# Kernel optimization log

Hardware: AMD Instinct MI355X
Metric: run time of the kernel (lower is better)

## Reference

```python
import jax, jax.numpy as jnp
import numpy as np
import math

STATE_DIM = 512
NUM_GROUPS = 32
VMD_MODES = 8
PERM_DIM = 4
MAX_PATTERNS = math.factorial(PERM_DIM)  # 24


def setup_inputs() -> dict:
    key = jax.random.key(0)
    B, T = 16, 4096
    hidden_states = jax.random.normal(key, (B, T, STATE_DIM), dtype=jnp.float32)
    return {"hidden_states": hidden_states}


def _vmd_decomposition(signals):
    # signals: [B, G, T] -> modes [B, G, K, T]
    B, G, T = signals.shape
    K = VMD_MODES
    fft_signal = jnp.fft.fft(signals, axis=2)
    freqs = jnp.fft.fftfreq(T).astype(jnp.float32)
    bandwidth = 1.0 / K
    center_freqs = jnp.linspace(-0.5, 0.5, K, dtype=jnp.float32)
    dist = jnp.abs(freqs[None, :] - center_freqs[:, None])          # [K, T]
    filters = jnp.exp(-0.5 * (dist / bandwidth) ** 2)
    filtered = fft_signal[:, :, None, :] * filters[None, None, :, :]
    return jnp.fft.ifft(filtered, axis=3).real.astype(jnp.float32)


def _pattern_ids(windows):
    # windows: [B, G, K, N, m] -> Lehmer-code pattern ids [B, G, K, N]
    m = windows.shape[-1]
    si = jnp.argsort(windows, axis=-1)
    fact = [math.factorial(j) for j in range(m)]
    pid = jnp.zeros(windows.shape[:-1], dtype=jnp.int32)
    for i in range(m - 1):
        smaller = (si[..., i:i + 1] > si[..., i + 1:]).sum(axis=-1).astype(jnp.int32)
        pid = pid + smaller * fact[m - 1 - i]
    return pid


def _tmptm(modes):
    # modes: [B, G, K, T] -> normalized transition histogram [B, G, MP^2]
    B, G, K, T = modes.shape
    m, MP = PERM_DIM, MAX_PATTERNS
    N = T - m + 1
    # unfold(3, m, 1): [B, G, K, N, m]
    windows = jnp.stack([modes[..., i:i + N] for i in range(m)], axis=-1)
    pid = _pattern_ids(windows)                       # [B, G, K, N]
    lin = pid[..., :-1] * MP + pid[..., 1:]           # [B, G, K, N-1]
    # fused scatter-add histogram over (K, N-1) per (B, G) -- replaces one_hot+sum
    offset = jnp.arange(B * G, dtype=jnp.int32).reshape(B, G, 1, 1) * (MP * MP)
    flat = (lin + offset).reshape(-1)
    counts = jnp.zeros(B * G * MP * MP, dtype=jnp.float32).at[flat].add(1.0)
    tmptm = counts.reshape(B, G, MP * MP)
    row_sums = jnp.maximum(tmptm.sum(axis=2, keepdims=True), 1.0)
    return tmptm / row_sums


def _fmptm(modes):
    # modes: [B, G, K, T] -> upper-triangular energy correlations [B, G, K*(K-1)/2]
    B, G, K, T = modes.shape
    energies = modes ** 2
    mean_e = energies.mean(axis=3, keepdims=True)
    std_e = jnp.maximum(energies.std(axis=3, keepdims=True, ddof=1), 1e-8)  # torch std is unbiased
    ne = (energies - mean_e) / std_e
    corr = jnp.einsum('bgkt,bglt->bgkl', ne, ne) / T
    iu, ju = jnp.triu_indices(K, k=1)
    return corr[:, :, iu, ju]


def reference(hidden_states):
    B, T, D = hidden_states.shape
    G = NUM_GROUPS
    spg = D // G
    hs = hidden_states.astype(jnp.float32)
    hs = hs.transpose(0, 2, 1).reshape(B, G, spg, T)
    group_pooled = hs.mean(axis=2)                    # [B, G, T]
    modes = _vmd_decomposition(group_pooled)          # [B, G, K, T]
    tmptm = _tmptm(modes)
    fmptm = _fmptm(modes)
    return tmptm, fmptm
```

## Files before the change

kernel.cpp:

```cpp
#include <hip/hip_runtime.h>
#include <hip/hip_fp16.h>

#define TT   4096
#define GG   32
#define NTH  512
#define SM_BYTES 101440

__device__ __forceinline__ float centerF(int k){
    return (float)(-0.5 + (double)k * (1.0/7.0));
}

__device__ __forceinline__ float filt(int m, float ck){
    float f = (float)((m < TT/2) ? m : (m - TT)) * (1.0f/(float)TT);
    float d = (f - ck) * 8.0f;
    return __expf(-0.5f * d * d);
}

__device__ __forceinline__ void fft_stage(const float* __restrict__ sr, const float* __restrict__ si,
                                          float* __restrict__ dr, float* __restrict__ di,
                                          int Ns, float sgn, int tid){
    const float PI_F = 3.14159265358979323846f;
#pragma unroll
    for (int u = 0; u < (TT/2)/NTH; ++u){
        int j = tid + u*NTH;
        float ar = sr[j],        ai = si[j];
        float br = sr[j+TT/2],   bi = si[j+TT/2];
        int   kk = j & (Ns-1);
        float ang = sgn * (PI_F * (float)kk / (float)Ns);
        float s, c;
        __sincosf(ang, &s, &c);
        float tr = br*c - bi*s;
        float ti = br*s + bi*c;
        int idxD = ((j & ~(Ns-1)) << 1) | kk;
        dr[idxD]     = ar + tr;  di[idxD]     = ai + ti;
        dr[idxD+Ns]  = ar - tr;  di[idxD+Ns]  = ai - ti;
    }
}

__device__ __forceinline__ void makeW(const float* __restrict__ Xr, const float* __restrict__ Xi,
                                      int m, float ck0, float ck1, float& wr, float& wi){
    int mm = (TT - m) & (TT - 1);
    float xr = Xr[m],  xi = Xi[m];
    float yr = Xr[mm], yi = Xi[mm];
    float f0m = filt(m, ck0), f0n = filt(mm, ck0);
    float f1m = filt(m, ck1), f1n = filt(mm, ck1);
    const float sc = 0.5f / (float)TT;
    float z0r = (xr*f0m + yr*f0n) * sc;
    float z0i = (xi*f0m - yi*f0n) * sc;
    float z1r = (xr*f1m + yr*f1n) * sc;
    float z1i = (xi*f1m - yi*f1n) * sc;
    wr = z0r - z1i;
    wi = z0i + z1r;
}

__device__ __forceinline__ int wt_of(int r){ return r==0 ? 6 : (r==1 ? 2 : (r==2 ? 1 : 0)); }

__device__ __forceinline__ int pattern_id(float v0, float v1, float v2, float v3){
    int c01 = (v0 <= v1), c02 = (v0 <= v2), c03 = (v0 <= v3);
    int c12 = (v1 <= v2), c13 = (v1 <= v3), c23 = (v2 <= v3);
    int r1 = c01 + (1-c12) + (1-c13);
    int r2 = c02 + c12 + (1-c23);
    int r3 = c03 + c13 + c23;
    int g1 = 1 - c01;
    int g2 = (1-c02) + (1-c12);
    int g3 = (1-c03) + (1-c13) + (1-c23);
    return wt_of(r1)*g1 + wt_of(r2)*g2 + wt_of(r3)*g3;
}

__device__ __forceinline__ void pattern_hist(const float* __restrict__ m, unsigned* __restrict__ hist, int tid){
    int start = tid * (TT / NTH);
    int endt  = start + (TT / NTH);
    if (endt > TT - 4) endt = TT - 4;
    float w0 = m[start], w1 = m[start+1], w2 = m[start+2], w3 = m[start+3];
    int prev = pattern_id(w0, w1, w2, w3);
    int cur = -1; unsigned cnt = 0;
    for (int t = start; t < endt; ++t){
        w0 = w1; w1 = w2; w2 = w3; w3 = m[t+4];
        int nxt = pattern_id(w0, w1, w2, w3);
        int lin = prev*24 + nxt;
        if (lin == cur) { cnt++; }
        else { if (cnt) atomicAdd(&hist[cur], cnt); cur = lin; cnt = 1; }
        prev = nxt;
    }
    if (cnt) atomicAdd(&hist[cur], cnt);
}

template<int P>
__device__ __forceinline__ void process_pair(int tid,
        const float* Xr, const float* Xi,
        float* Ar, float* Ai, float* Br, float* Bi,
        float (&ce)[6][8],
        unsigned* hist, float* redbuf, float* mu_s, float* diag_s, float* cm_s){
    const int k0 = 2*P, k1 = 2*P+1;
    const float ck0 = centerF(k0), ck1 = centerF(k1);

#pragma unroll
    for (int u = 0; u < (TT/2)/NTH; ++u){
        int j = tid + u*NTH;
        float war, wai, wbr, wbi;
        makeW(Xr, Xi, j,        ck0, ck1, war, wai);
        makeW(Xr, Xi, j + TT/2, ck0, ck1, wbr, wbi);
        Ar[2*j]   = war + wbr;  Ai[2*j]   = wai + wbi;
        Ar[2*j+1] = war - wbr;  Ai[2*j+1] = wai - wbi;
    }
    __syncthreads();
    for (int s = 2; s <= 12; ++s){
        int Ns = 1 << (s-1);
        if (s & 1) fft_stage(Br, Bi, Ar, Ai, Ns, 1.f, tid);
        else       fft_stage(Ar, Ai, Br, Bi, Ns, 1.f, tid);
        __syncthreads();
    }

    {
        float s0 = 0.f, s1 = 0.f;
#pragma unroll
        for (int u = 0; u < TT/NTH; ++u){
            int t = tid + u*NTH;
            float m0 = Br[t], m1 = Bi[t];
            s0 += m0*m0; s1 += m1*m1;
        }
        for (int off = 32; off > 0; off >>= 1){
            s0 += __shfl_down(s0, off);
            s1 += __shfl_down(s1, off);
        }
        int lane = tid & 63, wid = tid >> 6;
        if (lane == 0){ redbuf[wid*16+0] = s0; redbuf[wid*16+1] = s1; }
        __syncthreads();
        if (tid < 2){
            float acc = 0.f;
            for (int w = 0; w < 8; ++w) acc += redbuf[w*16 + tid];
            mu_s[k0 + tid] = acc * (1.0f/(float)TT);
        }
        __syncthreads();
    }

    pattern_hist(Br, hist, tid);
    pattern_hist(Bi, hist, tid);

    {
        const float mu0 = mu_s[k0], mu1 = mu_s[k1];
        float accd0 = 0.f, accd1 = 0.f, accx = 0.f;
        float accl[(4*P > 0) ? 4*P : 1];
#pragma unroll
        for (int i = 0; i < 4*P; ++i) accl[i] = 0.f;
#pragma unroll
        for (int u = 0; u < TT/NTH; ++u){
            int t = tid + u*NTH;
            float m0 = Br[t], m1 = Bi[t];
            float c0 = m0*m0 - mu0, c1 = m1*m1 - mu1;
            accd0 += c0*c0; accd1 += c1*c1; accx += c0*c1;
#pragma unroll
            for (int l = 0; l < 2*P; ++l){
                accl[2*l]   += ce[l][u] * c0;
                accl[2*l+1] += ce[l][u] * c1;
            }
            if (P < 3){ ce[k0][u] = c0; ce[k1][u] = c1; }
        }
        const int NACC = 3 + 4*P;
        float vals[NACC];
        vals[0] = accd0; vals[1] = accd1; vals[2] = accx;
#pragma unroll
        for (int i = 0; i < 4*P; ++i) vals[3+i] = accl[i];
#pragma unroll
        for (int a = 0; a < NACC; ++a){
            float v = vals[a];
            for (int off = 32; off > 0; off >>= 1) v += __shfl_down(v, off);
            if ((tid & 63) == 0) redbuf[(tid>>6)*16 + a] = v;
        }
        __syncthreads();
        if (tid < NACC){
            float acc = 0.f;
            for (int w = 0; w < 8; ++w) acc += redbuf[w*16 + tid];
            int a = tid;
            if      (a == 0) diag_s[k0] = acc;
            else if (a == 1) diag_s[k1] = acc;
            else if (a == 2) cm_s[k0*8 + k1] = acc;
            else {
                int l = (a-3) >> 1; int wch = (a-3) & 1;
                cm_s[l*8 + k0 + wch] = acc;
            }
        }
        __syncthreads();
    }
}

template<bool DIRECT>
__global__ __launch_bounds__(NTH, 1)
void fused_kernel(const float* __restrict__ hs, const float* __restrict__ pooled,
                  float* __restrict__ out){
    extern __shared__ float smem[];
    float* Xr = smem;
    float* Xi = Xr + TT;
    float* Ar = Xi + TT;
    float* Ai = Ar + TT;
    float* Br = Ai + TT;
    float* Bi = Br + TT;
    unsigned* hist = (unsigned*)(smem + 24576);
    float* redbuf  = smem + 24576 + 576;
    float* mu_s    = redbuf + 128;
    float* diag_s  = mu_s + 8;
    float* cm_s    = diag_s + 8;

    int tid = threadIdx.x;
    int bg  = blockIdx.x;
    int b   = bg >> 5, g = bg & 31;

    for (int i = tid; i < 576; i += NTH) hist[i] = 0u;

    if (DIRECT){
        const float* base = hs + ((size_t)b * TT) * 512 + g * 16;
#pragma unroll
        for (int u = 0; u < TT/NTH; ++u){
            int t = tid + u*NTH;
            const float4* p = (const float4*)(base + (size_t)t * 512);
            float4 a = p[0], bb = p[1], cc = p[2], dd = p[3];
            float s = a.x+a.y+a.z+a.w + bb.x+bb.y+bb.z+bb.w
                    + cc.x+cc.y+cc.z+cc.w + dd.x+dd.y+dd.z+dd.w;
            Xr[t] = s * (1.0f/16.0f);
            Xi[t] = 0.f;
        }
    } else {
        const float* pp = pooled + (size_t)bg * TT;
#pragma unroll
        for (int u = 0; u < TT/NTH; ++u){
            int t = tid + u*NTH;
            Xr[t] = pp[t];
            Xi[t] = 0.f;
        }
    }
    __syncthreads();

    for (int s = 1; s <= 12; ++s){
        int Ns = 1 << (s-1);
        if (s & 1) fft_stage(Xr, Xi, Ar, Ai, Ns, -1.f, tid);
        else       fft_stage(Ar, Ai, Xr, Xi, Ns, -1.f, tid);
        __syncthreads();
    }

    float ce[6][8];
    process_pair<0>(tid, Xr, Xi, Ar, Ai, Br, Bi, ce, hist, redbuf, mu_s, diag_s, cm_s);
    process_pair<1>(tid, Xr, Xi, Ar, Ai, Br, Bi, ce, hist, redbuf, mu_s, diag_s, cm_s);
    process_pair<2>(tid, Xr, Xi, Ar, Ai, Br, Bi, ce, hist, redbuf, mu_s, diag_s, cm_s);
    process_pair<3>(tid, Xr, Xi, Ar, Ai, Br, Bi, ce, hist, redbuf, mu_s, diag_s, cm_s);

    __syncthreads();

    float* tm_out = out + (size_t)bg * 576;
    for (int i = tid; i < 576; i += NTH)
        tm_out[i] = (float)hist[i] * (1.0f/32736.0f);

    if (tid < 28){
        int q = tid, k = 0, cnt = 7, rem = q;
        while (rem >= cnt){ rem -= cnt; k++; cnt--; }
        int l = k + 1 + rem;
        float sk = fmaxf(sqrtf(diag_s[k] * (1.0f/4095.0f)), 1e-8f);
        float sl = fmaxf(sqrtf(diag_s[l] * (1.0f/4095.0f)), 1e-8f);
        out[294912 + (size_t)bg*28 + q] = cm_s[k*8 + l] / (4096.0f * sk * sl);
    }
}

__global__ __launch_bounds__(256)
void pool_kernel(const float* __restrict__ hs, float* __restrict__ pooled){
    __shared__ float tile[32][65];
    int blk = blockIdx.x;
    int b   = blk >> 6;
    int t0  = (blk & 63) << 6;
    int tid = threadIdx.x;
    int lane = tid & 63, wid = tid >> 6;
#pragma unroll
    for (int i = 0; i < 16; ++i){
        int tl = wid + i*4;
        int t  = t0 + tl;
        const float4* p = (const float4*)(hs + ((size_t)b * TT + t) * 512);
        float4 a = p[lane];
        float4 c = p[lane + 64];
        float pa = a.x+a.y+a.z+a.w;
        float pc = c.x+c.y+c.z+c.w;
        pa += __shfl_xor(pa, 1); pa += __shfl_xor(pa, 2);
        pc += __shfl_xor(pc, 1); pc += __shfl_xor(pc, 2);
        if ((lane & 3) == 0){
            int gq = lane >> 2;
            tile[gq][tl]      = pa * (1.0f/16.0f);
            tile[gq + 16][tl] = pc * (1.0f/16.0f);
        }
    }
    __syncthreads();
    for (int idx = tid; idx < 2048; idx += 256){
        int g = idx >> 6, tt = idx & 63;
        pooled[((size_t)b * 32 + g) * TT + t0 + tt] = tile[g][tt];
    }
}

extern "C" void kernel_launch(void* const* d_in, const int* in_sizes, int n_in,
                              void* d_out, int out_size, void* d_ws, size_t ws_size,
                              hipStream_t stream){
    const float* hs = (const float*)d_in[0];
    float* out = (float*)d_out;
    const size_t poolBytes = (size_t)512 * TT * sizeof(float);

    if (d_ws && ws_size >= poolBytes){
        float* pooled = (float*)d_ws;
        pool_kernel<<<1024, 256, 0, stream>>>(hs, pooled);
        hipFuncSetAttribute((const void*)fused_kernel<false>,
                            hipFuncAttributeMaxDynamicSharedMemorySize, SM_BYTES);
        fused_kernel<false><<<512, NTH, SM_BYTES, stream>>>(hs, pooled, out);
    } else {
        hipFuncSetAttribute((const void*)fused_kernel<true>,
                            hipFuncAttributeMaxDynamicSharedMemorySize, SM_BYTES);
        fused_kernel<true><<<512, NTH, SM_BYTES, stream>>>(hs, nullptr, out);
    }
}
```

Baseline: 357.6 us.

## Rewrite fused VMD kernel with radix-4 FFT, padded LDS, fp16 energy cache

The FFT moves from radix-2 to radix-4 stages with twiddles precomputed once per thread, and the last forward stage is kept in registers. Spectral filtering uses a real symmetric filter gain instead of the old conjugate-pair construction. LDS arrays are padded to avoid bank conflicts, and shared memory shrinks from six arrays to four so more blocks fit per CU. Energy correlations switch to one pass over raw sums (sum and sum of products) with cross-mode energies cached as fp16 in registers, and pattern ids go through LDS into a double-banked histogram. The risks are precision loss from fp16 energies and one-pass variance, plus higher register pressure under the launch-bounds hint of 4.

```diff
diff --git a/kernel.cpp b/kernel.cpp
--- a/kernel.cpp
+++ b/kernel.cpp
@@ -2,55 +2,65 @@
 #include <hip/hip_fp16.h>
 
 #define TT   4096
-#define GG   32
 #define NTH  512
-#define SM_BYTES 101440
+#define ARR  4224
+#define SK(e) ((e) + ((e) >> 5))
+#define SM_FLOATS (4*ARR + 1152 + 44)
+#define SM_BYTES  (SM_FLOATS * 4)
 
 __device__ __forceinline__ float centerF(int k){
     return (float)(-0.5 + (double)k * (1.0/7.0));
 }
-
-__device__ __forceinline__ float filt(int m, float ck){
-    float f = (float)((m < TT/2) ? m : (m - TT)) * (1.0f/(float)TT);
+__device__ __forceinline__ float freq_of(int m){
+    return (float)((m < TT/2) ? m : (m - TT)) * (1.0f/(float)TT);
+}
+__device__ __forceinline__ float filtv(float f, float ck){
     float d = (f - ck) * 8.0f;
     return __expf(-0.5f * d * d);
 }
-
-__device__ __forceinline__ void fft_stage(const float* __restrict__ sr, const float* __restrict__ si,
-                                          float* __restrict__ dr, float* __restrict__ di,
-                                          int Ns, float sgn, int tid){
-    const float PI_F = 3.14159265358979323846f;
-#pragma unroll
-    for (int u = 0; u < (TT/2)/NTH; ++u){
-        int j = tid + u*NTH;
-        float ar = sr[j],        ai = si[j];
-        float br = sr[j+TT/2],   bi = si[j+TT/2];
-        int   kk = j & (Ns-1);
-        float ang = sgn * (PI_F * (float)kk / (float)Ns);
-        float s, c;
-        __sincosf(ang, &s, &c);
-        float tr = br*c - bi*s;
-        float ti = br*s + bi*c;
-        int idxD = ((j & ~(Ns-1)) << 1) | kk;
-        dr[idxD]     = ar + tr;  di[idxD]     = ai + ti;
-        dr[idxD+Ns]  = ar - tr;  di[idxD+Ns]  = ai - ti;
-    }
-}
-
-__device__ __forceinline__ void makeW(const float* __restrict__ Xr, const float* __restrict__ Xi,
-                                      int m, float ck0, float ck1, float& wr, float& wi){
+__device__ __forceinline__ float Gval(int m, float ck){
     int mm = (TT - m) & (TT - 1);
-    float xr = Xr[m],  xi = Xi[m];
-    float yr = Xr[mm], yi = Xi[mm];
-    float f0m = filt(m, ck0), f0n = filt(mm, ck0);
-    float f1m = filt(m, ck1), f1n = filt(mm, ck1);
-    const float sc = 0.5f / (float)TT;
-    float z0r = (xr*f0m + yr*f0n) * sc;
-    float z0i = (xi*f0m - yi*f0n) * sc;
-    float z1r = (xr*f1m + yr*f1n) * sc;
-    float z1i = (xi*f1m - yi*f1n) * sc;
-    wr = z0r - z1i;
-    wi = z0i + z1r;
+    return (filtv(freq_of(m), ck) + filtv(freq_of(mm), ck)) * (0.5f/(float)TT);
+}
+
+struct C4 { float r0,i0,r1,i1,r2,i2,r3,i3; };
+
+template<int SGN>
+__device__ __forceinline__ void bf4(float c0r,float c0i,float c1r,float c1i,
+                                    float c2r,float c2i,float c3r,float c3i,
+                                    float ur,float ui, C4& o){
+    float u2r = ur*ur - ui*ui, u2i = 2.f*ur*ui;
+    float u3r = u2r*ur - u2i*ui, u3i = u2r*ui + u2i*ur;
+    if (SGN < 0){ ui = -ui; u2i = -u2i; u3i = -u3i; }
+    float ar = u2r*c2r - u2i*c2i, ai = u2r*c2i + u2i*c2r;
+    float br = ur*c1r  - ui*c1i,  bi = ur*c1i  + ui*c1r;
+    float er = u3r*c3r - u3i*c3i, ei = u3r*c3i + u3i*c3r;
+    float s0r = c0r+ar, s0i = c0i+ai, s1r = c0r-ar, s1i = c0i-ai;
+    float s2r = br+er,  s2i = bi+ei,  s3r = br-er,  s3i = bi-ei;
+    o.r0 = s0r+s2r; o.i0 = s0i+s2i;
+    o.r2 = s0r-s2r; o.i2 = s0i-s2i;
+    if (SGN > 0){ o.r1 = s1r-s3i; o.i1 = s1i+s3r; o.r3 = s1r+s3i; o.i3 = s1i-s3r; }
+    else        { o.r1 = s1r+s3i; o.i1 = s1i-s3r; o.r3 = s1r-s3i; o.i3 = s1i+s3r; }
+}
+
+template<int SGN>
+__device__ __forceinline__ void stageLDS(const float* __restrict__ sr, const float* __restrict__ si,
+                                         float* __restrict__ dr, float* __restrict__ di,
+                                         int Ns, float uAr,float uAi,float uBr,float uBi, int tid){
+#pragma unroll
+    for (int h = 0; h < 2; ++h){
+        int j = tid + h*512;
+        float ur = h ? uBr : uAr, ui = h ? uBi : uAi;
+        int kk = j & (Ns-1);
+        int base = ((j & ~(Ns-1)) << 2) | kk;
+        C4 o;
+        bf4<SGN>(sr[SK(j)],si[SK(j)], sr[SK(j+1024)],si[SK(j+1024)],
+                 sr[SK(j+2048)],si[SK(j+2048)], sr[SK(j+3072)],si[SK(j+3072)], ur,ui,o);
+        dr[SK(base)]       = o.r0;  di[SK(base)]       = o.i0;
+        dr[SK(base+Ns)]    = o.r1;  di[SK(base+Ns)]    = o.i1;
+        dr[SK(base+2*Ns)]  = o.r2;  di[SK(base+2*Ns)]  = o.i2;
+        dr[SK(base+3*Ns)]  = o.r3;  di[SK(base+3*Ns)]  = o.i3;
+    }
 }
 
 __device__ __forceinline__ int wt_of(int r){ return r==0 ? 6 : (r==1 ? 2 : (r==2 ? 1 : 0)); }
@@ -67,195 +77,213 @@
     return wt_of(r1)*g1 + wt_of(r2)*g2 + wt_of(r3)*g3;
 }
 
-__device__ __forceinline__ void pattern_hist(const float* __restrict__ m, unsigned* __restrict__ hist, int tid){
-    int start = tid * (TT / NTH);
-    int endt  = start + (TT / NTH);
-    if (endt > TT - 4) endt = TT - 4;
-    float w0 = m[start], w1 = m[start+1], w2 = m[start+2], w3 = m[start+3];
-    int prev = pattern_id(w0, w1, w2, w3);
-    int cur = -1; unsigned cnt = 0;
-    for (int t = start; t < endt; ++t){
-        w0 = w1; w1 = w2; w2 = w3; w3 = m[t+4];
-        int nxt = pattern_id(w0, w1, w2, w3);
-        int lin = prev*24 + nxt;
-        if (lin == cur) { cnt++; }
-        else { if (cnt) atomicAdd(&hist[cur], cnt); cur = lin; cnt = 1; }
-        prev = nxt;
-    }
-    if (cnt) atomicAdd(&hist[cur], cnt);
+__device__ __forceinline__ int DIDX(int k, int l){
+    return 8 + k*8 + l - (k*(k+1))/2;
+}
+
+__device__ __forceinline__ void reduce_to(float v, float* res, int idx, int tid){
+#pragma unroll
+    for (int off = 32; off; off >>= 1) v += __shfl_xor(v, off);
+    if ((tid & 63) == 0) atomicAdd(&res[idx], v);
 }
 
 template<int P>
 __device__ __forceinline__ void process_pair(int tid,
-        const float* Xr, const float* Xi,
         float* Ar, float* Ai, float* Br, float* Bi,
-        float (&ce)[6][8],
-        unsigned* hist, float* redbuf, float* mu_s, float* diag_s, float* cm_s){
+        unsigned* hist, float* res,
+        const float (&xr)[8], const float (&xi)[8],
+        __half2 (&est)[6][4],
+        float t4r,float t4i,float t16r,float t16i,float t64r,float t64i,
+        float t256r,float t256i,float tAr,float tAi,float tBr,float tBi){
+    const float ck0 = centerF(2*P), ck1 = centerF(2*P+1);
+
+#pragma unroll
+    for (int h = 0; h < 2; ++h){
+        int j = tid + h*512;
+        float cr[4], ci[4];
+#pragma unroll
+        for (int q = 0; q < 4; ++q){
+            int v = 2*q + h;
+            int m = j + 1024*q;
+            float g0 = Gval(m, ck0), g1 = Gval(m, ck1);
+            cr[q] = xr[v]*g0 - xi[v]*g1;
+            ci[q] = xi[v]*g0 + xr[v]*g1;
+        }
+        C4 o; bf4<1>(cr[0],ci[0],cr[1],ci[1],cr[2],ci[2],cr[3],ci[3], 1.f,0.f, o);
+        int base = 4*j;
+        Ar[SK(base)]   = o.r0;  Ai[SK(base)]   = o.i0;
+        Ar[SK(base+1)] = o.r1;  Ai[SK(base+1)] = o.i1;
+        Ar[SK(base+2)] = o.r2;  Ai[SK(base+2)] = o.i2;
+        Ar[SK(base+3)] = o.r3;  Ai[SK(base+3)] = o.i3;
+    }
+    __syncthreads();
+    stageLDS<1>(Ar,Ai,Br,Bi,    4, t4r,t4i,t4r,t4i, tid);       __syncthreads();
+    stageLDS<1>(Br,Bi,Ar,Ai,   16, t16r,t16i,t16r,t16i, tid);   __syncthreads();
+    stageLDS<1>(Ar,Ai,Br,Bi,   64, t64r,t64i,t64r,t64i, tid);   __syncthreads();
+    stageLDS<1>(Br,Bi,Ar,Ai,  256, t256r,t256i,t256r,t256i, tid); __syncthreads();
+    stageLDS<1>(Ar,Ai,Br,Bi, 1024, tAr,tAi,tBr,tBi, tid);       __syncthreads();
+
+    int* pidR = (int*)Ar;
+    int* pidI = (int*)Ai;
+
+    float aS0=0.f, aS1=0.f, aD00=0.f, aD11=0.f, aD01=0.f;
+    float aX[(P > 0) ? 4*P : 1];
+#pragma unroll
+    for (int i = 0; i < ((P>0)?4*P:1); ++i) aX[i] = 0.f;
+
+    float carry0 = 0.f, carry1 = 0.f;
+#pragma unroll
+    for (int u = 0; u < 8; ++u){
+        int t  = tid + u*NTH;
+        int t1 = (t+1 < TT) ? t+1 : TT-1;
+        int t2 = (t+2 < TT) ? t+2 : TT-1;
+        int t3 = (t+3 < TT) ? t+3 : TT-1;
+        float b0 = Br[SK(t)], b1 = Br[SK(t1)], b2 = Br[SK(t2)], b3 = Br[SK(t3)];
+        float i0 = Bi[SK(t)], i1 = Bi[SK(t1)], i2 = Bi[SK(t2)], i3 = Bi[SK(t3)];
+        float e0 = b0*b0, e1 = i0*i0;
+        aS0 += e0; aS1 += e1;
+        aD00 += e0*e0; aD11 += e1*e1; aD01 += e0*e1;
+#pragma unroll
+        for (int l = 0; l < 2*P; ++l){
+            float el = (u & 1) ? __high2float(est[l][u>>1]) : __low2float(est[l][u>>1]);
+            aX[2*l]   += el * e0;
+            aX[2*l+1] += el * e1;
+        }
+        if constexpr (P < 3){
+            if ((u & 1) == 0){ carry0 = e0; carry1 = e1; }
+            else {
+                est[2*P][u>>1]   = __floats2half2_rn(carry0, e0);
+                est[2*P+1][u>>1] = __floats2half2_rn(carry1, e1);
+            }
+        }
+        if (t <= TT-4){
+            pidR[t] = pattern_id(b0,b1,b2,b3);
+            pidI[t] = pattern_id(i0,i1,i2,i3);
+        }
+    }
+    __syncthreads();
+
+    unsigned* h = hist + 576*((tid>>6) & 1);
+#pragma unroll
+    for (int u = 0; u < 8; ++u){
+        int t = tid + u*NTH;
+        if (t <= TT-5){
+            atomicAdd(&h[pidR[t]*24 + pidR[t+1]], 1u);
+            atomicAdd(&h[pidI[t]*24 + pidI[t+1]], 1u);
+        }
+    }
+    __syncthreads();
+
     const int k0 = 2*P, k1 = 2*P+1;
-    const float ck0 = centerF(k0), ck1 = centerF(k1);
-
-#pragma unroll
-    for (int u = 0; u < (TT/2)/NTH; ++u){
-        int j = tid + u*NTH;
-        float war, wai, wbr, wbi;
-        makeW(Xr, Xi, j,        ck0, ck1, war, wai);
-        makeW(Xr, Xi, j + TT/2, ck0, ck1, wbr, wbi);
-        Ar[2*j]   = war + wbr;  Ai[2*j]   = wai + wbi;
-        Ar[2*j+1] = war - wbr;  Ai[2*j+1] = wai - wbi;
-    }
-    __syncthreads();
-    for (int s = 2; s <= 12; ++s){
-        int Ns = 1 << (s-1);
-        if (s & 1) fft_stage(Br, Bi, Ar, Ai, Ns, 1.f, tid);
-        else       fft_stage(Ar, Ai, Br, Bi, Ns, 1.f, tid);
-        __syncthreads();
-    }
-
-    {
-        float s0 = 0.f, s1 = 0.f;
-#pragma unroll
-        for (int u = 0; u < TT/NTH; ++u){
-            int t = tid + u*NTH;
-            float m0 = Br[t], m1 = Bi[t];
-            s0 += m0*m0; s1 += m1*m1;
-        }
-        for (int off = 32; off > 0; off >>= 1){
-            s0 += __shfl_down(s0, off);
-            s1 += __shfl_down(s1, off);
-        }
-        int lane = tid & 63, wid = tid >> 6;
-        if (lane == 0){ redbuf[wid*16+0] = s0; redbuf[wid*16+1] = s1; }
-        __syncthreads();
-        if (tid < 2){
-            float acc = 0.f;
-            for (int w = 0; w < 8; ++w) acc += redbuf[w*16 + tid];
-            mu_s[k0 + tid] = acc * (1.0f/(float)TT);
-        }
-        __syncthreads();
-    }
-
-    pattern_hist(Br, hist, tid);
-    pattern_hist(Bi, hist, tid);
-
-    {
-        const float mu0 = mu_s[k0], mu1 = mu_s[k1];
-        float accd0 = 0.f, accd1 = 0.f, accx = 0.f;
-        float accl[(4*P > 0) ? 4*P : 1];
-#pragma unroll
-        for (int i = 0; i < 4*P; ++i) accl[i] = 0.f;
-#pragma unroll
-        for (int u = 0; u < TT/NTH; ++u){
-            int t = tid + u*NTH;
-            float m0 = Br[t], m1 = Bi[t];
-            float c0 = m0*m0 - mu0, c1 = m1*m1 - mu1;
-            accd0 += c0*c0; accd1 += c1*c1; accx += c0*c1;
-#pragma unroll
-            for (int l = 0; l < 2*P; ++l){
-                accl[2*l]   += ce[l][u] * c0;
-                accl[2*l+1] += ce[l][u] * c1;
-            }
-            if (P < 3){ ce[k0][u] = c0; ce[k1][u] = c1; }
-        }
-        const int NACC = 3 + 4*P;
-        float vals[NACC];
-        vals[0] = accd0; vals[1] = accd1; vals[2] = accx;
-#pragma unroll
-        for (int i = 0; i < 4*P; ++i) vals[3+i] = accl[i];
-#pragma unroll
-        for (int a = 0; a < NACC; ++a){
-            float v = vals[a];
-            for (int off = 32; off > 0; off >>= 1) v += __shfl_down(v, off);
-            if ((tid & 63) == 0) redbuf[(tid>>6)*16 + a] = v;
-        }
-        __syncthreads();
-        if (tid < NACC){
-            float acc = 0.f;
-            for (int w = 0; w < 8; ++w) acc += redbuf[w*16 + tid];
-            int a = tid;
-            if      (a == 0) diag_s[k0] = acc;
-            else if (a == 1) diag_s[k1] = acc;
-            else if (a == 2) cm_s[k0*8 + k1] = acc;
-            else {
-                int l = (a-3) >> 1; int wch = (a-3) & 1;
-                cm_s[l*8 + k0 + wch] = acc;
-            }
-        }
-        __syncthreads();
+    reduce_to(aS0,  res, k0, tid);
+    reduce_to(aS1,  res, k1, tid);
+    reduce_to(aD00, res, DIDX(k0,k0), tid);
+    reduce_to(aD11, res, DIDX(k1,k1), tid);
+    reduce_to(aD01, res, DIDX(k0,k1), tid);
+#pragma unroll
+    for (int l = 0; l < 2*P; ++l){
+        reduce_to(aX[2*l],   res, DIDX(l,k0), tid);
+        reduce_to(aX[2*l+1], res, DIDX(l,k1), tid);
     }
 }
 
 template<bool DIRECT>
-__global__ __launch_bounds__(NTH, 1)
+__global__ __launch_bounds__(NTH, 4)
 void fused_kernel(const float* __restrict__ hs, const float* __restrict__ pooled,
                   float* __restrict__ out){
     extern __shared__ float smem[];
-    float* Xr = smem;
-    float* Xi = Xr + TT;
-    float* Ar = Xi + TT;
-    float* Ai = Ar + TT;
-    float* Br = Ai + TT;
-    float* Bi = Br + TT;
-    unsigned* hist = (unsigned*)(smem + 24576);
-    float* redbuf  = smem + 24576 + 576;
-    float* mu_s    = redbuf + 128;
-    float* diag_s  = mu_s + 8;
-    float* cm_s    = diag_s + 8;
-
-    int tid = threadIdx.x;
-    int bg  = blockIdx.x;
-    int b   = bg >> 5, g = bg & 31;
-
-    for (int i = tid; i < 576; i += NTH) hist[i] = 0u;
+    float* Ar = smem;
+    float* Ai = smem + ARR;
+    float* Br = smem + 2*ARR;
+    float* Bi = smem + 3*ARR;
+    unsigned* hist = (unsigned*)(smem + 4*ARR);
+    float* res = smem + 4*ARR + 1152;
+
+    const int tid = threadIdx.x;
+    const int bg = blockIdx.x, b = bg >> 5, g = bg & 31;
+
+    for (int i = tid; i < 1152; i += NTH) hist[i] = 0u;
+    if (tid < 44) res[tid] = 0.f;
+
+    const float PI_F = 3.14159265358979323846f;
+    float t4r,t4i,t16r,t16i,t64r,t64i,t256r,t256i,tAr,tAi,tBr,tBi;
+    { float s,c;
+      __sincosf(PI_F*(float)(tid &   3)/   8.f, &s,&c); t4r=c;   t4i=s;
+      __sincosf(PI_F*(float)(tid &  15)/  32.f, &s,&c); t16r=c;  t16i=s;
+      __sincosf(PI_F*(float)(tid &  63)/ 128.f, &s,&c); t64r=c;  t64i=s;
+      __sincosf(PI_F*(float)(tid & 255)/ 512.f, &s,&c); t256r=c; t256i=s;
+      __sincosf(PI_F*(float)tid        /2048.f, &s,&c); tAr=c;   tAi=s;
+      __sincosf(PI_F*(float)(tid+512)  /2048.f, &s,&c); tBr=c;   tBi=s;
+    }
 
     if (DIRECT){
         const float* base = hs + ((size_t)b * TT) * 512 + g * 16;
 #pragma unroll
-        for (int u = 0; u < TT/NTH; ++u){
+        for (int u = 0; u < 8; ++u){
             int t = tid + u*NTH;
             const float4* p = (const float4*)(base + (size_t)t * 512);
             float4 a = p[0], bb = p[1], cc = p[2], dd = p[3];
             float s = a.x+a.y+a.z+a.w + bb.x+bb.y+bb.z+bb.w
                     + cc.x+cc.y+cc.z+cc.w + dd.x+dd.y+dd.z+dd.w;
-            Xr[t] = s * (1.0f/16.0f);
-            Xi[t] = 0.f;
+            Ar[SK(t)] = s * (1.0f/16.0f);
+            Ai[SK(t)] = 0.f;
         }
     } else {
         const float* pp = pooled + (size_t)bg * TT;
 #pragma unroll
-        for (int u = 0; u < TT/NTH; ++u){
+        for (int u = 0; u < 8; ++u){
             int t = tid + u*NTH;
-            Xr[t] = pp[t];
-            Xi[t] = 0.f;
-        }
-    }
-    __syncthreads();
-
-    for (int s = 1; s <= 12; ++s){
-        int Ns = 1 << (s-1);
-        if (s & 1) fft_stage(Xr, Xi, Ar, Ai, Ns, -1.f, tid);
-        else       fft_stage(Ar, Ai, Xr, Xi, Ns, -1.f, tid);
-        __syncthreads();
-    }
-
-    float ce[6][8];
-    process_pair<0>(tid, Xr, Xi, Ar, Ai, Br, Bi, ce, hist, redbuf, mu_s, diag_s, cm_s);
-    process_pair<1>(tid, Xr, Xi, Ar, Ai, Br, Bi, ce, hist, redbuf, mu_s, diag_s, cm_s);
-    process_pair<2>(tid, Xr, Xi, Ar, Ai, Br, Bi, ce, hist, redbuf, mu_s, diag_s, cm_s);
-    process_pair<3>(tid, Xr, Xi, Ar, Ai, Br, Bi, ce, hist, redbuf, mu_s, diag_s, cm_s);
-
-    __syncthreads();
-
-    float* tm_out = out + (size_t)bg * 576;
+            Ar[SK(t)] = pp[t];
+            Ai[SK(t)] = 0.f;
+        }
+    }
+    __syncthreads();
+
+    stageLDS<-1>(Ar,Ai,Br,Bi,   1, 1.f,0.f,1.f,0.f, tid);        __syncthreads();
+    stageLDS<-1>(Br,Bi,Ar,Ai,   4, t4r,t4i,t4r,t4i, tid);        __syncthreads();
+    stageLDS<-1>(Ar,Ai,Br,Bi,  16, t16r,t16i,t16r,t16i, tid);    __syncthreads();
+    stageLDS<-1>(Br,Bi,Ar,Ai,  64, t64r,t64i,t64r,t64i, tid);    __syncthreads();
+    stageLDS<-1>(Ar,Ai,Br,Bi, 256, t256r,t256i,t256r,t256i, tid);__syncthreads();
+
+    float xr[8], xi[8];
+    {
+        C4 o;
+        bf4<-1>(Br[SK(tid)],Bi[SK(tid)], Br[SK(tid+1024)],Bi[SK(tid+1024)],
+                Br[SK(tid+2048)],Bi[SK(tid+2048)], Br[SK(tid+3072)],Bi[SK(tid+3072)],
+                tAr,tAi,o);
+        xr[0]=o.r0; xi[0]=o.i0; xr[2]=o.r1; xi[2]=o.i1;
+        xr[4]=o.r2; xi[4]=o.i2; xr[6]=o.r3; xi[6]=o.i3;
+        bf4<-1>(Br[SK(tid+512)],Bi[SK(tid+512)], Br[SK(tid+1536)],Bi[SK(tid+1536)],
+                Br[SK(tid+2560)],Bi[SK(tid+2560)], Br[SK(tid+3584)],Bi[SK(tid+3584)],
+                tBr,tBi,o);
+        xr[1]=o.r0; xi[1]=o.i0; xr[3]=o.r1; xi[3]=o.i1;
+        xr[5]=o.r2; xi[5]=o.i2; xr[7]=o.r3; xi[7]=o.i3;
+    }
+
+    __half2 est[6][4];
+    process_pair<0>(tid,Ar,Ai,Br,Bi,hist,res,xr,xi,est,t4r,t4i,t16r,t16i,t64r,t64i,t256r,t256i,tAr,tAi,tBr,tBi);
+    process_pair<1>(tid,Ar,Ai,Br,Bi,hist,res,xr,xi,est,t4r,t4i,t16r,t16i,t64r,t64i,t256r,t256i,tAr,tAi,tBr,tBi);
+    process_pair<2>(tid,Ar,Ai,Br,Bi,hist,res,xr,xi,est,t4r,t4i,t16r,t16i,t64r,t64i,t256r,t256i,tAr,tAi,tBr,tBi);
+    process_pair<3>(tid,Ar,Ai,Br,Bi,hist,res,xr,xi,est,t4r,t4i,t16r,t16i,t64r,t64i,t256r,t256i,tAr,tAi,tBr,tBi);
+
+    __syncthreads();
+
+    float* tm = out + (size_t)bg * 576;
     for (int i = tid; i < 576; i += NTH)
-        tm_out[i] = (float)hist[i] * (1.0f/32736.0f);
+        tm[i] = (float)(hist[i] + hist[i+576]) * (1.0f/32736.0f);
 
     if (tid < 28){
         int q = tid, k = 0, cnt = 7, rem = q;
         while (rem >= cnt){ rem -= cnt; k++; cnt--; }
         int l = k + 1 + rem;
-        float sk = fmaxf(sqrtf(diag_s[k] * (1.0f/4095.0f)), 1e-8f);
-        float sl = fmaxf(sqrtf(diag_s[l] * (1.0f/4095.0f)), 1e-8f);
-        out[294912 + (size_t)bg*28 + q] = cm_s[k*8 + l] / (4096.0f * sk * sl);
+        float Sk = res[k], Sl = res[l];
+        float Dkl = res[DIDX(k,l)], Dkk = res[DIDX(k,k)], Dll = res[DIDX(l,l)];
+        float cov = Dkl - Sk*Sl*(1.0f/4096.0f);
+        float vk = (Dkk - Sk*Sk*(1.0f/4096.0f)) * (1.0f/4095.0f);
+        float vl = (Dll - Sl*Sl*(1.0f/4096.0f)) * (1.0f/4095.0f);
+        float sk = fmaxf(sqrtf(fmaxf(vk, 0.f)), 1e-8f);
+        float sl = fmaxf(sqrtf(fmaxf(vl, 0.f)), 1e-8f);
+        out[294912 + (size_t)bg*28 + q] = cov * (1.0f/4096.0f) / (sk*sl);
     }
 }
 
```

Result: faster. 307.3 us (-14.1%).
